# Optimization experiments

Hardware: AMD Instinct MI355X
Metric: run time of the kernel (lower is better)

## Reference

```python
import jax, jax.numpy as jnp
import numpy as np

MAX_AGENTS = 64
IN_DIM = 256
HID_DIM = 512
OUT_DIM = 256
MAX_CHILDREN = 8
BATCH = 1024


def setup_inputs() -> dict:
    key = jax.random.key(0)
    k1, k2, k3, k4, k5 = jax.random.split(key, 5)
    W1 = jax.random.normal(k1, (MAX_AGENTS, IN_DIM, HID_DIM), dtype=jnp.float32) * 0.02
    b1 = jnp.zeros((MAX_AGENTS, HID_DIM), dtype=jnp.float32)
    W2 = jax.random.normal(k2, (MAX_AGENTS, HID_DIM, OUT_DIM), dtype=jnp.float32) * 0.02
    b2 = jnp.zeros((MAX_AGENTS, OUT_DIM), dtype=jnp.float32)
    router_weights = jax.random.normal(k3, (MAX_AGENTS, HID_DIM, MAX_CHILDREN), dtype=jnp.float32) * 0.01
    agent_indices = jax.random.randint(k4, (BATCH,), 0, MAX_AGENTS, dtype=jnp.int64 if jax.config.jax_enable_x64 else jnp.int32)
    x = jax.random.normal(k5, (BATCH, IN_DIM), dtype=jnp.float32)
    return {
        "x": x,
        "W1": W1,
        "b1": b1,
        "W2": W2,
        "b2": b2,
        "router_weights": router_weights,
        "agent_indices": agent_indices,
    }


def reference(x, W1, b1, W2, b2, router_weights, agent_indices):
    # Gather per-sample weights (same as torch advanced indexing W1[agent_indices])
    w1 = W1[agent_indices]           # [B, In, Hid]
    b1g = b1[agent_indices]          # [B, Hid]
    w2 = W2[agent_indices]           # [B, Hid, Out]
    b2g = b2[agent_indices]          # [B, Out]
    rw = router_weights[agent_indices]  # [B, Hid, C]

    # per-sample MLP: bmm with a singleton row -> einsum
    h = jax.nn.relu(jnp.einsum('bi,bih->bh', x, w1) + b1g)      # [B, Hid]
    out = jnp.einsum('bh,bho->bo', h, w2) + b2g                 # [B, Out]
    r_logits = jnp.einsum('bh,bhc->bc', h, rw)                  # [B, C]
    return (h, out, r_logits)
```

## Files before the change

kernel.cpp:

```cpp
#include <hip/hip_runtime.h>

#define IN_DIM   256
#define HID_DIM  512
#define OUT_DIM  256
#define N_CHILD  8
#define BATCH    1024

#define SB    16
#define PAD   20
#define MAXCH 128
#define CK    128

extern "C" __global__ __launch_bounds__(1024)
void prep_sort(const int* __restrict__ raw, int* __restrict__ sorted,
               int* __restrict__ ch_agent, int* __restrict__ ch_start,
               int* __restrict__ ch_len)
{
    __shared__ int cnt[64], start[64];
    __shared__ int is32;
    const int t = threadIdx.x;
    if (t < 64) cnt[t] = 0;
    if (t == 0) is32 = 0;
    __syncthreads();
    if (raw[2 * (t & 511) + 1] != 0) is32 = 1;
    __syncthreads();
    const int a = (is32 ? raw[t] : raw[2 * t]) & 63;
    atomicAdd(&cnt[a], 1);
    __syncthreads();
    if (t == 0) {
        int off = 0, nch = 0;
        for (int i = 0; i < 64; ++i) {
            start[i] = off;
            const int c = cnt[i];
            for (int p = 0; p < c; p += SB) {
                ch_agent[nch] = i;
                ch_start[nch] = off + p;
                ch_len[nch]   = (c - p < SB) ? (c - p) : SB;
                ++nch;
            }
            off += c;
        }
        for (; nch < MAXCH; ++nch) ch_len[nch] = 0;
    }
    __syncthreads();
    if (t < 64) cnt[t] = 0;
    __syncthreads();
    const int pos = start[a] + atomicAdd(&cnt[a], 1);
    sorted[pos] = t;
}

extern "C" __global__ __launch_bounds__(256)
void k1_mlp1(const float* __restrict__ x, const float* __restrict__ W1,
             const float* __restrict__ b1,
             const int* __restrict__ sorted, const int* __restrict__ ch_agent,
             const int* __restrict__ ch_start, const int* __restrict__ ch_len,
             float* __restrict__ h_out)
{
    const int chunk = blockIdx.x;
    const int len = ch_len[chunk];
    if (len == 0) return;
    const int a  = ch_agent[chunk];
    const int cs = ch_start[chunk];
    const int t  = threadIdx.x;
    const int bcol = blockIdx.y * 64;

    __shared__ float xsT[IN_DIM * PAD];
    __shared__ float wS[CK * 64];
    __shared__ int   sidS[SB];

    if (t < SB) sidS[t] = sorted[cs + (t < len ? t : len - 1)];
    __syncthreads();
    #pragma unroll
    for (int s = 0; s < SB; ++s)
        xsT[t * PAD + s] = x[(size_t)sidS[s] * IN_DIM + t];

    const int cg = t & 15;
    const int sg = (t >> 4) & 1;
    const int kq = t >> 5;
    const float* Wb = W1 + (size_t)a * IN_DIM * HID_DIM + bcol;

    float acc[4][8];
    #pragma unroll
    for (int j = 0; j < 4; ++j)
        #pragma unroll
        for (int i = 0; i < 8; ++i) acc[j][i] = 0.f;

    for (int p = 0; p < IN_DIM / CK; ++p) {
        const int k0 = p * CK;
        __syncthreads();
        #pragma unroll
        for (int i = 0; i < 8; ++i) {
            const int id  = t + i * 256;
            const int row = id >> 4;
            const int c4  = (id & 15) * 4;
            const float4 w = *(const float4*)(Wb + (size_t)(k0 + row) * HID_DIM + c4);
            *(float4*)(&wS[row * 64 + c4]) = w;
        }
        __syncthreads();
        #pragma unroll 4
        for (int i = 0; i < CK / 8; ++i) {
            const int kl = kq * (CK / 8) + i;
            const float4 w  = *(const float4*)(&wS[kl * 64 + cg * 4]);
            const float4 xa = *(const float4*)(&xsT[(k0 + kl) * PAD + sg * 8]);
            const float4 xb = *(const float4*)(&xsT[(k0 + kl) * PAD + sg * 8 + 4]);
            const float wv[4] = {w.x, w.y, w.z, w.w};
            const float xv[8] = {xa.x, xa.y, xa.z, xa.w, xb.x, xb.y, xb.z, xb.w};
            #pragma unroll
            for (int j = 0; j < 4; ++j)
                #pragma unroll
                for (int q = 0; q < 8; ++q)
                    acc[j][q] = fmaf(wv[j], xv[q], acc[j][q]);
        }
    }

    __syncthreads();
    float* sc = wS;
    #pragma unroll
    for (int j = 0; j < 4; ++j)
        #pragma unroll
        for (int i = 0; i < 8; ++i)
            sc[t * 32 + j * 8 + i] = acc[j][i];
    __syncthreads();
    const int c = t & 63;
    #pragma unroll
    for (int u = 0; u < 4; ++u) {
        const int s = (t >> 6) + u * 4;
        float v = 0.f;
        #pragma unroll
        for (int q = 0; q < 8; ++q)
            v += sc[((c >> 2) + ((s >> 3) << 4) + (q << 5)) * 32
                    + (c & 3) * 8 + (s & 7)];
        v = fmaxf(v + b1[a * HID_DIM + bcol + c], 0.f);
        h_out[(size_t)sidS[s] * HID_DIM + bcol + c] = v;
    }
}

extern "C" __global__ __launch_bounds__(256)
void k2_mlp2(const float* __restrict__ h, const float* __restrict__ W2,
             const float* __restrict__ b2,
             const int* __restrict__ sorted, const int* __restrict__ ch_agent,
             const int* __restrict__ ch_start, const int* __restrict__ ch_len,
             float* __restrict__ o_out)
{
    const int chunk = blockIdx.x;
    const int len = ch_len[chunk];
    if (len == 0) return;
    const int a  = ch_agent[chunk];
    const int cs = ch_start[chunk];
    const int t  = threadIdx.x;
    const int bcol = blockIdx.y * 64;

    __shared__ float hsT[CK * PAD];
    __shared__ float wS[CK * 64];
    __shared__ int   sidS[SB];

    if (t < SB) sidS[t] = sorted[cs + (t < len ? t : len - 1)];
    __syncthreads();

    const int cg = t & 15;
    const int sg = (t >> 4) & 1;
    const int kq = t >> 5;
    const float* Wb = W2 + (size_t)a * HID_DIM * OUT_DIM + bcol;

    float acc[4][8];
    #pragma unroll
    for (int j = 0; j < 4; ++j)
        #pragma unroll
        for (int i = 0; i < 8; ++i) acc[j][i] = 0.f;

    for (int p = 0; p < HID_DIM / CK; ++p) {
        const int k0 = p * CK;
        __syncthreads();
        {
            const int row = t & 127;
            const int sh  = t >> 7;
            #pragma unroll
            for (int i = 0; i < 8; ++i) {
                const int s = sh * 8 + i;
                hsT[row * PAD + s] = h[(size_t)sidS[s] * HID_DIM + k0 + row];
            }
        }
        #pragma unroll
        for (int i = 0; i < 8; ++i) {
            const int id  = t + i * 256;
            const int row = id >> 4;
            const int c4  = (id & 15) * 4;
            const float4 w = *(const float4*)(Wb + (size_t)(k0 + row) * OUT_DIM + c4);
            *(float4*)(&wS[row * 64 + c4]) = w;
        }
        __syncthreads();
        #pragma unroll 4
        for (int i = 0; i < CK / 8; ++i) {
            const int kl = kq * (CK / 8) + i;
            const float4 w  = *(const float4*)(&wS[kl * 64 + cg * 4]);
            const float4 xa = *(const float4*)(&hsT[kl * PAD + sg * 8]);
            const float4 xb = *(const float4*)(&hsT[kl * PAD + sg * 8 + 4]);
            const float wv[4] = {w.x, w.y, w.z, w.w};
            const float xv[8] = {xa.x, xa.y, xa.z, xa.w, xb.x, xb.y, xb.z, xb.w};
            #pragma unroll
            for (int j = 0; j < 4; ++j)
                #pragma unroll
                for (int q = 0; q < 8; ++q)
                    acc[j][q] = fmaf(wv[j], xv[q], acc[j][q]);
        }
    }

    __syncthreads();
    float* sc = wS;
    #pragma unroll
    for (int j = 0; j < 4; ++j)
        #pragma unroll
        for (int i = 0; i < 8; ++i)
            sc[t * 32 + j * 8 + i] = acc[j][i];
    __syncthreads();
    const int c = t & 63;
    #pragma unroll
    for (int u = 0; u < 4; ++u) {
        const int s = (t >> 6) + u * 4;
        float v = 0.f;
        #pragma unroll
        for (int q = 0; q < 8; ++q)
            v += sc[((c >> 2) + ((s >> 3) << 4) + (q << 5)) * 32
                    + (c & 3) * 8 + (s & 7)];
        v += b2[a * OUT_DIM + bcol + c];
        o_out[(size_t)sidS[s] * OUT_DIM + bcol + c] = v;
    }
}

extern "C" __global__ __launch_bounds__(256)
void k3_router(const float* __restrict__ h, const float* __restrict__ rw,
               const int* __restrict__ sorted, const int* __restrict__ ch_agent,
               const int* __restrict__ ch_start, const int* __restrict__ ch_len,
               float* __restrict__ r_out)
{
    const int chunk = blockIdx.x;
    const int len = ch_len[chunk];
    if (len == 0) return;
    const int a  = ch_agent[chunk];
    const int cs = ch_start[chunk];
    const int t  = threadIdx.x;

    __shared__ float sc[256];
    __shared__ int   sidS[SB];
    if (t < SB) sidS[t] = sorted[cs + (t < len ? t : len - 1)];
    __syncthreads();

    const int c  = t & 7;
    const int s  = (t >> 3) & 15;
    const int kq = t >> 7;
    const float* hv = h  + (size_t)sidS[s] * HID_DIM + kq * 256;
    const float* rv = rw + (size_t)a * HID_DIM * N_CHILD
                          + (size_t)kq * 256 * N_CHILD + c;
    float p = 0.f;
    #pragma unroll 8
    for (int k = 0; k < 256; ++k)
        p = fmaf(hv[k], rv[(size_t)k * N_CHILD], p);
    sc[t] = p;
    __syncthreads();
    if (t < 128)
        r_out[(size_t)sidS[s] * N_CHILD + c] = sc[t] + sc[t + 128];
}

extern "C" void kernel_launch(void* const* d_in, const int* in_sizes, int n_in,
                              void* d_out, int out_size, void* d_ws, size_t ws_size,
                              hipStream_t stream) {
    const float* x  = (const float*)d_in[0];
    const float* W1 = (const float*)d_in[1];
    const float* b1 = (const float*)d_in[2];
    const float* W2 = (const float*)d_in[3];
    const float* b2 = (const float*)d_in[4];
    const float* rw = (const float*)d_in[5];
    const int* raw  = (const int*)d_in[6];

    int* ws       = (int*)d_ws;
    int* sorted   = ws;
    int* ch_agent = ws + 1024;
    int* ch_start = ws + 1152;
    int* ch_len   = ws + 1280;

    float* out   = (float*)d_out;
    float* h_out = out;
    float* o_out = h_out + (size_t)BATCH * HID_DIM;
    float* r_out = o_out + (size_t)BATCH * OUT_DIM;

    hipLaunchKernelGGL(prep_sort, dim3(1), dim3(1024), 0, stream,
                       raw, sorted, ch_agent, ch_start, ch_len);
    hipLaunchKernelGGL(k1_mlp1, dim3(MAXCH, 8), dim3(256), 0, stream,
                       x, W1, b1, sorted, ch_agent, ch_start, ch_len, h_out);
    hipLaunchKernelGGL(k2_mlp2, dim3(MAXCH, 4), dim3(256), 0, stream,
                       h_out, W2, b2, sorted, ch_agent, ch_start, ch_len, o_out);
    hipLaunchKernelGGL(k3_router, dim3(MAXCH), dim3(256), 0, stream,
                       h_out, rw, sorted, ch_agent, ch_start, ch_len, r_out);
}
```

Before: 155.3 us.

## Enlarge per-block sample chunks and tile, reduce partial sums via warp shuffles

Raises the number of samples per chunk from 16 to 32 so each weight tile loaded from global memory is reused across more samples, cutting weight traffic. Each thread now computes an 8x8 register tile with the K dimension split across lanes, and the partial sums are combined with shuffle-xor instead of a shared-memory scratch pass. Groups of 8 samples beyond the chunk length skip the FMA work. The router kernel drops its split-K shared reduction and uses float4 loads of h. In exchange, chunks become coarser, the 64-float accumulators raise register pressure and may lower occupancy, and the prep_sort chunking (hidden) must match the new SB/MAXCH.

```diff
diff --git a/kernel.cpp b/kernel.cpp
--- a/kernel.cpp
+++ b/kernel.cpp
@@ -6,10 +6,9 @@
 #define N_CHILD  8
 #define BATCH    1024
 
-#define SB    16
-#define PAD   20
-#define MAXCH 128
-#define CK    128
+#define SB    32
+#define XPAD  36
+#define MAXCH 96
 
 extern "C" __global__ __launch_bounds__(1024)
 void prep_sort(const int* __restrict__ raw, int* __restrict__ sorted,
@@ -62,76 +61,89 @@
     const int a  = ch_agent[chunk];
     const int cs = ch_start[chunk];
     const int t  = threadIdx.x;
-    const int bcol = blockIdx.y * 64;
-
-    __shared__ float xsT[IN_DIM * PAD];
-    __shared__ float wS[CK * 64];
+    const int bcol = blockIdx.y * 128;
+
+    __shared__ float xsT[64 * XPAD];
+    __shared__ float wS[64 * 128];
     __shared__ int   sidS[SB];
 
     if (t < SB) sidS[t] = sorted[cs + (t < len ? t : len - 1)];
     __syncthreads();
+
+    const int cg = t & 15;
+    const int kq = (t >> 4) & 3;
+    const int sg = t >> 6;
+    const bool act = (sg * 8) < len;
+    const float* Wb = W1 + (size_t)a * IN_DIM * HID_DIM + bcol;
+
+    float acc[64];
     #pragma unroll
-    for (int s = 0; s < SB; ++s)
-        xsT[t * PAD + s] = x[(size_t)sidS[s] * IN_DIM + t];
-
-    const int cg = t & 15;
-    const int sg = (t >> 4) & 1;
-    const int kq = t >> 5;
-    const float* Wb = W1 + (size_t)a * IN_DIM * HID_DIM + bcol;
-
-    float acc[4][8];
-    #pragma unroll
-    for (int j = 0; j < 4; ++j)
-        #pragma unroll
-        for (int i = 0; i < 8; ++i) acc[j][i] = 0.f;
-
-    for (int p = 0; p < IN_DIM / CK; ++p) {
-        const int k0 = p * CK;
+    for (int i = 0; i < 64; ++i) acc[i] = 0.f;
+
+    for (int p = 0; p < IN_DIM / 64; ++p) {
+        const int k0 = p * 64;
         __syncthreads();
+        {
+            const int kr = t & 63;
+            const int sb = (t >> 6) * 8;
+            #pragma unroll
+            for (int i = 0; i < 8; ++i)
+                xsT[kr * XPAD + sb + i] =
+                    x[(size_t)sidS[sb + i] * IN_DIM + k0 + kr];
+        }
         #pragma unroll
         for (int i = 0; i < 8; ++i) {
             const int id  = t + i * 256;
-            const int row = id >> 4;
-            const int c4  = (id & 15) * 4;
-            const float4 w = *(const float4*)(Wb + (size_t)(k0 + row) * HID_DIM + c4);
-            *(float4*)(&wS[row * 64 + c4]) = w;
+            const int row = id >> 5;
+            const int c4  = (id & 31) * 4;
+            *(float4*)(&wS[row * 128 + c4]) =
+                *(const float4*)(Wb + (size_t)(k0 + row) * HID_DIM + c4);
         }
         __syncthreads();
-        #pragma unroll 4
-        for (int i = 0; i < CK / 8; ++i) {
-            const int kl = kq * (CK / 8) + i;
-            const float4 w  = *(const float4*)(&wS[kl * 64 + cg * 4]);
-            const float4 xa = *(const float4*)(&xsT[(k0 + kl) * PAD + sg * 8]);
-            const float4 xb = *(const float4*)(&xsT[(k0 + kl) * PAD + sg * 8 + 4]);
-            const float wv[4] = {w.x, w.y, w.z, w.w};
-            const float xv[8] = {xa.x, xa.y, xa.z, xa.w, xb.x, xb.y, xb.z, xb.w};
-            #pragma unroll
-            for (int j = 0; j < 4; ++j)
+        if (act) {
+            #pragma unroll
+            for (int i = 0; i < 16; ++i) {
+                const int row = i * 4 + kq;
+                const float4 w0 = *(const float4*)(&wS[row * 128 + cg * 4]);
+                const float4 w1 = *(const float4*)(&wS[row * 128 + 64 + cg * 4]);
+                const float4 xa = *(const float4*)(&xsT[row * XPAD + sg * 8]);
+                const float4 xb = *(const float4*)(&xsT[row * XPAD + sg * 8 + 4]);
+                const float wv[8] = {w0.x, w0.y, w0.z, w0.w, w1.x, w1.y, w1.z, w1.w};
+                const float xv[8] = {xa.x, xa.y, xa.z, xa.w, xb.x, xb.y, xb.z, xb.w};
                 #pragma unroll
-                for (int q = 0; q < 8; ++q)
-                    acc[j][q] = fmaf(wv[j], xv[q], acc[j][q]);
-        }
-    }
-
-    __syncthreads();
-    float* sc = wS;
-    #pragma unroll
-    for (int j = 0; j < 4; ++j)
+                for (int c = 0; c < 8; ++c)
+                    #pragma unroll
+                    for (int s = 0; s < 8; ++s)
+                        acc[c * 8 + s] = fmaf(wv[c], xv[s], acc[c * 8 + s]);
+            }
+        }
+    }
+
+    if (act) {
         #pragma unroll
-        for (int i = 0; i < 8; ++i)
-            sc[t * 32 + j * 8 + i] = acc[j][i];
-    __syncthreads();
-    const int c = t & 63;
-    #pragma unroll
-    for (int u = 0; u < 4; ++u) {
-        const int s = (t >> 6) + u * 4;
-        float v = 0.f;
-        #pragma unroll
-        for (int q = 0; q < 8; ++q)
-            v += sc[((c >> 2) + ((s >> 3) << 4) + (q << 5)) * 32
-                    + (c & 3) * 8 + (s & 7)];
-        v = fmaxf(v + b1[a * HID_DIM + bcol + c], 0.f);
-        h_out[(size_t)sidS[s] * HID_DIM + bcol + c] = v;
+        for (int i = 0; i < 64; ++i) {
+            acc[i] += __shfl_xor(acc[i], 16);
+            acc[i] += __shfl_xor(acc[i], 32);
+        }
+        if (kq == 0) {
+            const float4 bA = *(const float4*)(b1 + a * HID_DIM + bcol + cg * 4);
+            const float4 bB = *(const float4*)(b1 + a * HID_DIM + bcol + 64 + cg * 4);
+            #pragma unroll
+            for (int s = 0; s < 8; ++s) {
+                float* hp = h_out + (size_t)sidS[sg * 8 + s] * HID_DIM + bcol;
+                float4 v0, v1;
+                v0.x = fmaxf(acc[0 * 8 + s] + bA.x, 0.f);
+                v0.y = fmaxf(acc[1 * 8 + s] + bA.y, 0.f);
+                v0.z = fmaxf(acc[2 * 8 + s] + bA.z, 0.f);
+                v0.w = fmaxf(acc[3 * 8 + s] + bA.w, 0.f);
+                v1.x = fmaxf(acc[4 * 8 + s] + bB.x, 0.f);
+                v1.y = fmaxf(acc[5 * 8 + s] + bB.y, 0.f);
+                v1.z = fmaxf(acc[6 * 8 + s] + bB.z, 0.f);
+                v1.w = fmaxf(acc[7 * 8 + s] + bB.w, 0.f);
+                *(float4*)(hp + cg * 4)      = v0;
+                *(float4*)(hp + 64 + cg * 4) = v1;
+            }
+        }
     }
 }
 
@@ -150,80 +162,88 @@
     const int t  = threadIdx.x;
     const int bcol = blockIdx.y * 64;
 
-    __shared__ float hsT[CK * PAD];
-    __shared__ float wS[CK * 64];
+    __shared__ float hsT[64 * XPAD];
+    __shared__ float wS[64 * 64];
     __shared__ int   sidS[SB];
 
     if (t < SB) sidS[t] = sorted[cs + (t < len ? t : len - 1)];
     __syncthreads();
 
-    const int cg = t & 15;
-    const int sg = (t >> 4) & 1;
-    const int kq = t >> 5;
+    const int cg = t & 7;
+    const int kq = (t >> 3) & 7;
+    const int sg = t >> 6;
+    const bool act = (sg * 8) < len;
     const float* Wb = W2 + (size_t)a * HID_DIM * OUT_DIM + bcol;
 
-    float acc[4][8];
+    float acc[64];
     #pragma unroll
-    for (int j = 0; j < 4; ++j)
-        #pragma unroll
-        for (int i = 0; i < 8; ++i) acc[j][i] = 0.f;
-
-    for (int p = 0; p < HID_DIM / CK; ++p) {
-        const int k0 = p * CK;
+    for (int i = 0; i < 64; ++i) acc[i] = 0.f;
+
+    for (int p = 0; p < HID_DIM / 64; ++p) {
+        const int k0 = p * 64;
         __syncthreads();
         {
-            const int row = t & 127;
-            const int sh  = t >> 7;
-            #pragma unroll
-            for (int i = 0; i < 8; ++i) {
-                const int s = sh * 8 + i;
-                hsT[row * PAD + s] = h[(size_t)sidS[s] * HID_DIM + k0 + row];
-            }
+            const int kr = t & 63;
+            const int sb = (t >> 6) * 8;
+            #pragma unroll
+            for (int i = 0; i < 8; ++i)
+                hsT[kr * XPAD + sb + i] =
+                    h[(size_t)sidS[sb + i] * HID_DIM + k0 + kr];
         }
         #pragma unroll
-        for (int i = 0; i < 8; ++i) {
+        for (int i = 0; i < 4; ++i) {
             const int id  = t + i * 256;
             const int row = id >> 4;
             const int c4  = (id & 15) * 4;
-            const float4 w = *(const float4*)(Wb + (size_t)(k0 + row) * OUT_DIM + c4);
-            *(float4*)(&wS[row * 64 + c4]) = w;
+            *(float4*)(&wS[row * 64 + c4]) =
+                *(const float4*)(Wb + (size_t)(k0 + row) * OUT_DIM + c4);
         }
         __syncthreads();
-        #pragma unroll 4
-        for (int i = 0; i < CK / 8; ++i) {
-            const int kl = kq * (CK / 8) + i;
-            const float4 w  = *(const float4*)(&wS[kl * 64 + cg * 4]);
-            const float4 xa = *(const float4*)(&hsT[kl * PAD + sg * 8]);
-            const float4 xb = *(const float4*)(&hsT[kl * PAD + sg * 8 + 4]);
-            const float wv[4] = {w.x, w.y, w.z, w.w};
-            const float xv[8] = {xa.x, xa.y, xa.z, xa.w, xb.x, xb.y, xb.z, xb.w};
-            #pragma unroll
-            for (int j = 0; j < 4; ++j)
+        if (act) {
+            #pragma unroll
+            for (int i = 0; i < 8; ++i) {
+                const int row = i * 8 + kq;
+                const float4 w0 = *(const float4*)(&wS[row * 64 + cg * 4]);
+                const float4 w1 = *(const float4*)(&wS[row * 64 + 32 + cg * 4]);
+                const float4 xa = *(const float4*)(&hsT[row * XPAD + sg * 8]);
+                const float4 xb = *(const float4*)(&hsT[row * XPAD + sg * 8 + 4]);
+                const float wv[8] = {w0.x, w0.y, w0.z, w0.w, w1.x, w1.y, w1.z, w1.w};
+                const float xv[8] = {xa.x, xa.y, xa.z, xa.w, xb.x, xb.y, xb.z, xb.w};
                 #pragma unroll
-                for (int q = 0; q < 8; ++q)
-                    acc[j][q] = fmaf(wv[j], xv[q], acc[j][q]);
-        }
-    }
-
-    __syncthreads();
-    float* sc = wS;
-    #pragma unroll
-    for (int j = 0; j < 4; ++j)
+                for (int c = 0; c < 8; ++c)
+                    #pragma unroll
+                    for (int s = 0; s < 8; ++s)
+                        acc[c * 8 + s] = fmaf(wv[c], xv[s], acc[c * 8 + s]);
+            }
+        }
+    }
+
+    if (act) {
         #pragma unroll
-        for (int i = 0; i < 8; ++i)
-            sc[t * 32 + j * 8 + i] = acc[j][i];
-    __syncthreads();
-    const int c = t & 63;
-    #pragma unroll
-    for (int u = 0; u < 4; ++u) {
-        const int s = (t >> 6) + u * 4;
-        float v = 0.f;
-        #pragma unroll
-        for (int q = 0; q < 8; ++q)
-            v += sc[((c >> 2) + ((s >> 3) << 4) + (q << 5)) * 32
-                    + (c & 3) * 8 + (s & 7)];
-        v += b2[a * OUT_DIM + bcol + c];
-        o_out[(size_t)sidS[s] * OUT_DIM + bcol + c] = v;
+        for (int i = 0; i < 64; ++i) {
+            acc[i] += __shfl_xor(acc[i], 8);
+            acc[i] += __shfl_xor(acc[i], 16);
+            acc[i] += __shfl_xor(acc[i], 32);
+        }
+        if (kq == 0) {
+            const float4 bA = *(const float4*)(b2 + a * OUT_DIM + bcol + cg * 4);
+            const float4 bB = *(const float4*)(b2 + a * OUT_DIM + bcol + 32 + cg * 4);
+            #pragma unroll
+            for (int s = 0; s < 8; ++s) {
+                float* op = o_out + (size_t)sidS[sg * 8 + s] * OUT_DIM + bcol;
+                float4 v0, v1;
+                v0.x = acc[0 * 8 + s] + bA.x;
+                v0.y = acc[1 * 8 + s] + bA.y;
+                v0.z = acc[2 * 8 + s] + bA.z;
+                v0.w = acc[3 * 8 + s] + bA.w;
+                v1.x = acc[4 * 8 + s] + bB.x;
+                v1.y = acc[5 * 8 + s] + bB.y;
+                v1.z = acc[6 * 8 + s] + bB.z;
+                v1.w = acc[7 * 8 + s] + bB.w;
+                *(float4*)(op + cg * 4)      = v0;
+                *(float4*)(op + 32 + cg * 4) = v1;
+            }
+        }
     }
 }
 
@@ -240,25 +260,24 @@
     const int cs = ch_start[chunk];
     const int t  = threadIdx.x;
 
-    __shared__ float sc[256];
-    __shared__ int   sidS[SB];
+    __shared__ int sidS[SB];
     if (t < SB) sidS[t] = sorted[cs + (t < len ? t : len - 1)];
     __syncthreads();
 
-    const int c  = t & 7;
-    const int s  = (t >> 3) & 15;
-    const int kq = t >> 7;
-    const float* hv = h  + (size_t)sidS[s] * HID_DIM + kq * 256;
-    const float* rv = rw + (size_t)a * HID_DIM * N_CHILD
-                          + (size_t)kq * 256 * N_CHILD + c;
+    const int c = t & 7;
+    const int s = t >> 3;
+    const float* hv = h  + (size_t)sidS[s] * HID_DIM;
+    const float* rv = rw + (size_t)a * HID_DIM * N_CHILD + c;
     float p = 0.f;
-    #pragma unroll 8
-    for (int k = 0; k < 256; ++k)
-        p = fmaf(hv[k], rv[(size_t)k * N_CHILD], p);
-    sc[t] = p;
-    __syncthreads();
-    if (t < 128)
-        r_out[(size_t)sidS[s] * N_CHILD + c] = sc[t] + sc[t + 128];
+    #pragma unroll 4
+    for (int k4 = 0; k4 < HID_DIM / 4; ++k4) {
+        const float4 hx = *(const float4*)(hv + k4 * 4);
+        p = fmaf(hx.x, rv[(size_t)(k4 * 4 + 0) * N_CHILD], p);
+        p = fmaf(hx.y, rv[(size_t)(k4 * 4 + 1) * N_CHILD], p);
+        p = fmaf(hx.z, rv[(size_t)(k4 * 4 + 2) * N_CHILD], p);
+        p = fmaf(hx.w, rv[(size_t)(k4 * 4 + 3) * N_CHILD], p);
+    }
+    r_out[(size_t)sidS[s] * N_CHILD + c] = p;
 }
 
 extern "C" void kernel_launch(void* const* d_in, const int* in_sizes, int n_in,
@@ -275,8 +294,8 @@
     int* ws       = (int*)d_ws;
     int* sorted   = ws;
     int* ch_agent = ws + 1024;
-    int* ch_start = ws + 1152;
-    int* ch_len   = ws + 1280;
+    int* ch_start = ws + 1120;
+    int* ch_len   = ws + 1216;
 
     float* out   = (float*)d_out;
     float* h_out = out;
@@ -285,7 +304,7 @@
 
     hipLaunchKernelGGL(prep_sort, dim3(1), dim3(1024), 0, stream,
                        raw, sorted, ch_agent, ch_start, ch_len);
-    hipLaunchKernelGGL(k1_mlp1, dim3(MAXCH, 8), dim3(256), 0, stream,
+    hipLaunchKernelGGL(k1_mlp1, dim3(MAXCH, 4), dim3(256), 0, stream,
                        x, W1, b1, sorted, ch_agent, ch_start, ch_len, h_out);
     hipLaunchKernelGGL(k2_mlp2, dim3(MAXCH, 4), dim3(256), 0, stream,
                        h_out, W2, b2, sorted, ch_agent, ch_start, ch_len, o_out);
```

New measurement: 175.7 us. 13.2% more time.
